# Kernel optimization log

Measured on AMD Instinct MI355X. Metric: run time of the kernel, lower is better.

## Reference

```python
import jax, jax.numpy as jnp
import numpy as np

B, T, D, HD = 8, 2048, 768, 64

def setup_inputs() -> dict:
    key = jax.random.key(0)
    k1, k2, k3, k4 = jax.random.split(key, 4)
    scale = 1.0 / np.sqrt(D)
    return {
        "x": jax.random.normal(k1, (B, T, D), dtype=jnp.float32),
        "Wq": jax.random.normal(k2, (D, HD), dtype=jnp.float32) * scale,
        "Wk": jax.random.normal(k3, (D, HD), dtype=jnp.float32) * scale,
        "Wv": jax.random.normal(k4, (D, HD), dtype=jnp.float32) * scale,
    }

def reference(x, Wq, Wk, Wv):
    # q,k,v: [B,T,HD]
    q = jnp.einsum('btd,dh->bth', x, Wq)
    k = jnp.einsum('btd,dh->bth', x, Wk)
    v = jnp.einsum('btd,dh->bth', x, Wv)
    dk = q.shape[-1]
    # scores: [B,T,T], scaled then causally masked with -inf
    scores = jnp.einsum('bqh,bkh->bqk', q, k) / jnp.sqrt(jnp.float32(dk))
    Tq = scores.shape[-1]
    causal = jnp.tril(jnp.ones((Tq, Tq), dtype=bool))
    scores = jnp.where(causal, scores, -jnp.inf)
    attn = jax.nn.softmax(scores, axis=-1)  # dropout rate 0 (eval mode)
    return jnp.einsum('bqk,bkh->bqh', attn, v)
```

## Files before the change

### kernel.cpp

```cpp
#include <hip/hip_runtime.h>
#include <hip/hip_bf16.h>
#include <stdint.h>

#define B_  8
#define T_  2048
#define D_  768
#define HD_ 64
#define M_  (B_ * T_)

typedef short s16x8 __attribute__((ext_vector_type(8)));
typedef float f32x4 __attribute__((ext_vector_type(4)));
typedef float f32x16 __attribute__((ext_vector_type(16)));
typedef unsigned int u32;

union Frag { uint4 u; s16x8 h; };

__device__ __forceinline__ unsigned short f2bf(float f) {
    unsigned u = __builtin_bit_cast(unsigned, f);
    u += 0x7FFFu + ((u >> 16) & 1u);
    return (unsigned short)(u >> 16);
}
__device__ __forceinline__ unsigned pack_bf16x2(float lo, float hi) {
    return (unsigned)f2bf(lo) | ((unsigned)f2bf(hi) << 16);
}
__device__ __forceinline__ unsigned cvt_pk(float lo, float hi) {
    unsigned r;
    asm("v_cvt_pk_bf16_f32 %0, %1, %2" : "=v"(r) : "v"(lo), "v"(hi));
    return r;
}

__device__ __forceinline__ void gl_lds16(const void* g, void* l) {
    __builtin_amdgcn_global_load_lds(
        (const __attribute__((address_space(1))) u32*)g,
        (__attribute__((address_space(3))) u32*)l, 16, 0, 0);
}

__global__ __launch_bounds__(64) void prep_pk(const float* __restrict__ Wq,
                                              const float* __restrict__ Wk,
                                              const float* __restrict__ Wv,
                                              unsigned short* __restrict__ pk) {
    int nb = blockIdx.x / 24, kk = blockIdx.x % 24;
    int lane = threadIdx.x, g = lane >> 4, t = lane & 15;
    int mat = nb >> 2, col = (nb & 3) * 16 + t;
    const float* W = (mat == 0) ? Wq : (mat == 1) ? Wk : Wv;
    float s = (mat == 0) ? 0.18033688011112042f : 1.0f;
    float v[8];
#pragma unroll
    for (int e = 0; e < 8; e++)
        v[e] = W[(size_t)(kk * 32 + g * 8 + e) * HD_ + col] * s;
    uint4 u;
    u.x = pack_bf16x2(v[0], v[1]);
    u.y = pack_bf16x2(v[2], v[3]);
    u.z = pack_bf16x2(v[4], v[5]);
    u.w = pack_bf16x2(v[6], v[7]);
    *(uint4*)(pk + ((size_t)blockIdx.x * 64 + lane) * 8) = u;
}

__global__ __launch_bounds__(256, 2) void qkv_proj(const float* __restrict__ x,
                                                   const unsigned short* __restrict__ pk,
                                                   unsigned short* __restrict__ qo,
                                                   unsigned short* __restrict__ ko,
                                                   unsigned short* __restrict__ vt) {
    __shared__ char xs[4][8192];

    int tid = threadIdx.x, w = tid >> 6, lane = tid & 63;
    int g = lane >> 4, t = lane & 15;
    int m0 = blockIdx.x * 32;

    auto STAGE = [&](int jb) {
        int buf = jb & 3;
#pragma unroll
        for (int h = 0; h < 2; h++) {
            int s = tid + h * 256;
            int row = s >> 4;
            int a = (s & 15) ^ (row & 15);
            gl_lds16(x + (size_t)(m0 + row) * D_ + jb * 64 + a * 4,
                     &xs[buf][(w * 64 + h * 256) * 16]);
        }
    };

    const unsigned short* wp = pk + (size_t)w * 36864;
    auto LOADB = [&](Frag (&bb)[6], int jb) {
#pragma unroll
        for (int j = 0; j < 3; j++)
#pragma unroll
            for (int c = 0; c < 2; c++)
                bb[j * 2 + c].u = *(const uint4*)(wp + ((size_t)(j * 24 + jb * 2 + c) * 64 + lane) * 8);
    };

    f32x4 acc[3][2];
#pragma unroll
    for (int j = 0; j < 3; j++)
#pragma unroll
        for (int mf = 0; mf < 2; mf++) acc[j][mf] = (f32x4){0.f, 0.f, 0.f, 0.f};

    Frag bfr[3][6];
    LOADB(bfr[0], 0);
    LOADB(bfr[1], 1);
    STAGE(0); STAGE(1); STAGE(2);

#pragma unroll
    for (int jb = 0; jb < 12; jb++) {
        if (jb + 2 < 12) LOADB(bfr[(jb + 2) % 3], jb + 2);
        if (jb == 0)       asm volatile("s_waitcnt vmcnt(10)" ::: "memory");
        else if (jb == 10) asm volatile("s_waitcnt vmcnt(8)"  ::: "memory");
        else if (jb == 11) asm volatile("s_waitcnt vmcnt(0)"  ::: "memory");
        else               asm volatile("s_waitcnt vmcnt(16)" ::: "memory");
        __builtin_amdgcn_s_barrier();
        int buf = jb & 3;

        Frag af[2][2];
#pragma unroll
        for (int mf = 0; mf < 2; mf++) {
            int r32 = mf * 16 + t;
#pragma unroll
            for (int c = 0; c < 2; c++) {
                float4 f0 = *(const float4*)(&xs[buf][r32 * 256 + (((c * 8 + g * 2 + 0) ^ t) * 16)]);
                float4 f1 = *(const float4*)(&xs[buf][r32 * 256 + (((c * 8 + g * 2 + 1) ^ t) * 16)]);
                af[mf][c].u.x = cvt_pk(f0.x, f0.y);
                af[mf][c].u.y = cvt_pk(f0.z, f0.w);
                af[mf][c].u.z = cvt_pk(f1.x, f1.y);
                af[mf][c].u.w = cvt_pk(f1.z, f1.w);
            }
        }
        __builtin_amdgcn_s_setprio(1);
#pragma unroll
        for (int j = 0; j < 3; j++)
#pragma unroll
            for (int c = 0; c < 2; c++) {
                acc[j][0] = __builtin_amdgcn_mfma_f32_16x16x32_bf16(af[0][c].h, bfr[jb % 3][j * 2 + c].h, acc[j][0], 0, 0, 0);
                acc[j][1] = __builtin_amdgcn_mfma_f32_16x16x32_bf16(af[1][c].h, bfr[jb % 3][j * 2 + c].h, acc[j][1], 0, 0, 0);
            }
        __builtin_amdgcn_s_setprio(0);
        __builtin_amdgcn_s_barrier();
        if (jb + 3 < 12) STAGE(jb + 3);
    }

#pragma unroll
    for (int j = 0; j < 3; j++) {
        int nb = w * 3 + j;
        int col = (nb & 3) * 16 + t;
#pragma unroll
        for (int mf = 0; mf < 2; mf++) {
            int row0 = m0 + mf * 16;
            if (nb < 8) {
                unsigned short* dst = (nb < 4) ? qo : ko;
#pragma unroll
                for (int r = 0; r < 4; r++)
                    dst[(size_t)(row0 + g * 4 + r) * HD_ + col] = f2bf(acc[j][mf][r]);
            } else {
                int bb = m0 >> 11;
                int trow = (row0 & 2047) + g * 4;
                uint2 pkk;
                pkk.x = cvt_pk(acc[j][mf][0], acc[j][mf][1]);
                pkk.y = cvt_pk(acc[j][mf][2], acc[j][mf][3]);
                *(uint2*)(vt + (((size_t)(bb * HD_ + col)) << 11) + trow) = pkk;
            }
        }
    }
}

__global__ __launch_bounds__(256) void attn(const unsigned short* __restrict__ qw,
                                            const unsigned short* __restrict__ kw,
                                            const unsigned short* __restrict__ vt,
                                            float* __restrict__ out) {
    __shared__ char smem[65536];

    int tid = threadIdx.x, wv = tid >> 6, lane = tid & 63;
    int hi = lane >> 5, l31 = lane & 31;
    int blk = blockIdx.x;
    int b = blk & 7, idx = blk >> 3;
    int qblk = (idx < 32) ? (63 - idx) : (idx - 32);
    int q0 = qblk * 32;
    int qg = q0 + l31;
    size_t bbase = (size_t)b * T_;
    int nt = qblk + 1;
    int ks = wv;
    int mt = (nt > ks) ? ((nt - ks + 3) >> 2) : 0;

    const unsigned short* kp = kw + bbase * HD_;
    const unsigned short* vp = vt + ((size_t)(b * HD_) << 11);
    char* KV = smem + wv * 16384;

    Frag qf[4];
#pragma unroll
    for (int c = 0; c < 4; c++)
        qf[c].u = *(const uint4*)(qw + (bbase + qg) * HD_ + c * 16 + hi * 8);

    auto STAGE = [&](int j, int buf) {
        int kv0 = j * 32;
#pragma unroll
        for (int q = 0; q < 4; q++) {
            int kr = q * 8 + (lane >> 3);
            int ka = (lane & 7) ^ (kr & 7);
            gl_lds16(kp + (size_t)(kv0 + kr) * HD_ + ka * 8, KV + buf * 4096 + q * 1024);
        }
#pragma unroll
        for (int q = 0; q < 4; q++) {
            int vd = q * 16 + (lane >> 2);
            int va = (lane & 3) ^ (vd & 3) ^ ((vd >> 2) & 3);
            gl_lds16(vp + ((size_t)vd << 11) + kv0 + va * 8, KV + 8192 + buf * 4096 + q * 1024);
        }
    };

    f32x16 o0, o1;
#pragma unroll
    for (int r = 0; r < 16; r++) { o0[r] = 0.f; o1[r] = 0.f; }
    float lacc = 0.f;

    if (mt > 0) STAGE(ks, 0);
    if (mt > 1) STAGE(ks + 4, 1);

#pragma unroll 1
    for (int i = 0; i < mt; i++) {
        if (i + 1 < mt) asm volatile("s_waitcnt vmcnt(8)" ::: "memory");
        else            asm volatile("s_waitcnt vmcnt(0)" ::: "memory");
        int j = ks + 4 * i;
        const char* KB = KV + (i & 1) * 4096;
        const char* VB = KV + 8192 + (i & 1) * 4096;
        int kv0 = j * 32;

        f32x16 st;
#pragma unroll
        for (int r = 0; r < 16; r++) st[r] = 0.f;
        __builtin_amdgcn_s_setprio(1);
#pragma unroll
        for (int c = 0; c < 4; c++) {
            Frag ka;
            ka.u = *(const uint4*)(KB + l31 * 128 + (((c * 2 + hi) ^ (l31 & 7)) * 16));
            st = __builtin_amdgcn_mfma_f32_32x32x16_bf16(ka.h, qf[c].h, st, 0, 0, 0);
        }
        __builtin_amdgcn_s_setprio(0);

        if (j == qblk) {
#pragma unroll
            for (int r = 0; r < 16; r++) {
                int key = kv0 + (r & 3) + 8 * (r >> 2) + 4 * hi;
                if (key > qg) st[r] = -1e30f;
            }
        }

        float p[16], ss = 0.f;
#pragma unroll
        for (int r = 0; r < 16; r++) { p[r] = exp2f(st[r]); ss += p[r]; }
        lacc += ss;

        u32 A0 = cvt_pk(p[0], p[1]),   A1 = cvt_pk(p[2], p[3]);
        u32 B0 = cvt_pk(p[4], p[5]),   B1 = cvt_pk(p[6], p[7]);
        u32 C0 = cvt_pk(p[8], p[9]),   C1 = cvt_pk(p[10], p[11]);
        u32 D0 = cvt_pk(p[12], p[13]), D1 = cvt_pk(p[14], p[15]);
        u32 A0x = (u32)__shfl_xor((int)A0, 32);
        u32 A1x = (u32)__shfl_xor((int)A1, 32);
        u32 B0x = (u32)__shfl_xor((int)B0, 32);
        u32 B1x = (u32)__shfl_xor((int)B1, 32);
        u32 C0x = (u32)__shfl_xor((int)C0, 32);
        u32 C1x = (u32)__shfl_xor((int)C1, 32);
        u32 D0x = (u32)__shfl_xor((int)D0, 32);
        u32 D1x = (u32)__shfl_xor((int)D1, 32);
        Frag pf0, pf1;
        pf0.u.x = hi ? B0x : A0;
        pf0.u.y = hi ? B1x : A1;
        pf0.u.z = hi ? B0  : A0x;
        pf0.u.w = hi ? B1  : A1x;
        pf1.u.x = hi ? D0x : C0;
        pf1.u.y = hi ? D1x : C1;
        pf1.u.z = hi ? D0  : C0x;
        pf1.u.w = hi ? D1  : C1x;

        __builtin_amdgcn_s_setprio(1);
        {
            int sw0 = (l31 & 3) ^ ((l31 >> 2) & 3);
            Frag va;
            va.u = *(const uint4*)(VB + l31 * 64 + (((hi) ^ sw0) * 16));
            o0 = __builtin_amdgcn_mfma_f32_32x32x16_bf16(va.h, pf0.h, o0, 0, 0, 0);
            va.u = *(const uint4*)(VB + l31 * 64 + (((2 + hi) ^ sw0) * 16));
            o0 = __builtin_amdgcn_mfma_f32_32x32x16_bf16(va.h, pf1.h, o0, 0, 0, 0);
            int d1 = 32 + l31;
            int sw1 = (d1 & 3) ^ ((d1 >> 2) & 3);
            va.u = *(const uint4*)(VB + d1 * 64 + (((hi) ^ sw1) * 16));
            o1 = __builtin_amdgcn_mfma_f32_32x32x16_bf16(va.h, pf0.h, o1, 0, 0, 0);
            va.u = *(const uint4*)(VB + d1 * 64 + (((2 + hi) ^ sw1) * 16));
            o1 = __builtin_amdgcn_mfma_f32_32x32x16_bf16(va.h, pf1.h, o1, 0, 0, 0);
        }
        __builtin_amdgcn_s_setprio(0);

        if (i + 2 < mt) STAGE(ks + 4 * (i + 2), i & 1);
    }

    __syncthreads();

    lacc += __shfl_xor(lacc, 32);
    float* MO = (float*)smem;
    if (wv) {
        int base = ((wv - 1) * 64 + lane) * 33;
#pragma unroll
        for (int r = 0; r < 16; r++) { MO[base + r] = o0[r]; MO[base + 16 + r] = o1[r]; }
        MO[base + 32] = lacc;
    }
    __syncthreads();
    if (wv == 0) {
        float ls = lacc;
#pragma unroll
        for (int k = 0; k < 3; k++) ls += MO[(k * 64 + lane) * 33 + 32];
        float inv = 1.0f / ls;
        float* op = out + (bbase + qg) * HD_;
#pragma unroll
        for (int r = 0; r < 16; r++) {
            float s0 = o0[r], s1 = o1[r];
#pragma unroll
            for (int k = 0; k < 3; k++) {
                s0 += MO[(k * 64 + lane) * 33 + r];
                s1 += MO[(k * 64 + lane) * 33 + 16 + r];
            }
            int dr = (r & 3) + 8 * (r >> 2) + 4 * hi;
            op[dr] = s0 * inv;
            op[32 + dr] = s1 * inv;
        }
    }
}

extern "C" void kernel_launch(void* const* d_in, const int* in_sizes, int n_in,
                              void* d_out, int out_size, void* d_ws, size_t ws_size,
                              hipStream_t stream) {
    const float* x  = (const float*)d_in[0];
    const float* Wq = (const float*)d_in[1];
    const float* Wk = (const float*)d_in[2];
    const float* Wv = (const float*)d_in[3];
    char* ws = (char*)d_ws;
    unsigned short* pkw = (unsigned short*)ws;
    unsigned short* qw = (unsigned short*)(ws + 294912);
    unsigned short* kw = (unsigned short*)(ws + 294912 + 2097152);
    unsigned short* vt = (unsigned short*)(ws + 294912 + 4194304);
    float* out = (float*)d_out;

    hipLaunchKernelGGL(prep_pk, dim3(288), dim3(64), 0, stream, Wq, Wk, Wv, pkw);
    hipLaunchKernelGGL(qkv_proj, dim3(M_ / 32), dim3(256), 0, stream, x, pkw, qw, kw, vt);
    hipLaunchKernelGGL(attn, dim3(512), dim3(256), 0, stream, qw, kw, vt, out);
}
```

Before: 45.13 us.

## Unroll the KV loop by two and overlap the next QK MFMA with softmax

The attention loop is split into a QK lambda and a softmax-plus-PV lambda, and the main loop is unrolled by two. The second tile's QK MFMAs are issued before the first tile's softmax and PV, so matrix work can overlap with exp and shuffle work. The single vmcnt wait per tile becomes finer waits that release the K half of each tile before its V half, with a tail path for odd tile counts. In exchange it needs more live registers for the second score tile, which may hurt occupancy, and it relies on the hand-counted vmcnt values staying correct.

```diff
diff --git a/kernel.cpp b/kernel.cpp
--- a/kernel.cpp
+++ b/kernel.cpp
@@ -208,19 +208,7 @@
     for (int r = 0; r < 16; r++) { o0[r] = 0.f; o1[r] = 0.f; }
     float lacc = 0.f;
 
-    if (mt > 0) STAGE(ks, 0);
-    if (mt > 1) STAGE(ks + 4, 1);
-
-#pragma unroll 1
-    for (int i = 0; i < mt; i++) {
-        if (i + 1 < mt) asm volatile("s_waitcnt vmcnt(8)" ::: "memory");
-        else            asm volatile("s_waitcnt vmcnt(0)" ::: "memory");
-        int j = ks + 4 * i;
-        const char* KB = KV + (i & 1) * 4096;
-        const char* VB = KV + 8192 + (i & 1) * 4096;
-        int kv0 = j * 32;
-
-        f32x16 st;
+    auto QK = [&](const char* KB, f32x16& st) {
 #pragma unroll
         for (int r = 0; r < 16; r++) st[r] = 0.f;
         __builtin_amdgcn_s_setprio(1);
@@ -231,7 +219,10 @@
             st = __builtin_amdgcn_mfma_f32_32x32x16_bf16(ka.h, qf[c].h, st, 0, 0, 0);
         }
         __builtin_amdgcn_s_setprio(0);
-
+    };
+
+    auto SMPV = [&](f32x16& st, int j, const char* VB) {
+        int kv0 = j * 32;
         if (j == qblk) {
 #pragma unroll
             for (int r = 0; r < 16; r++) {
@@ -239,7 +230,6 @@
                 if (key > qg) st[r] = -1e30f;
             }
         }
-
         float p[16], ss = 0.f;
 #pragma unroll
         for (int r = 0; r < 16; r++) { p[r] = exp2f(st[r]); ss += p[r]; }
@@ -283,10 +273,44 @@
             o1 = __builtin_amdgcn_mfma_f32_32x32x16_bf16(va.h, pf1.h, o1, 0, 0, 0);
         }
         __builtin_amdgcn_s_setprio(0);
-
+    };
+
+    if (mt > 0) STAGE(ks, 0);
+    if (mt > 1) STAGE(ks + 4, 1);
+
+    int i = 0;
+#pragma unroll 1
+    for (; i + 2 <= mt; i += 2) {
+        int ja = ks + 4 * i, jb2 = ja + 4;
+        const char* KA = KV + (i & 1) * 4096;
+        const char* VA = KV + 8192 + (i & 1) * 4096;
+        const char* KB2 = KV + ((i + 1) & 1) * 4096;
+        const char* VB2 = KV + 8192 + ((i + 1) & 1) * 4096;
+
+        asm volatile("s_waitcnt vmcnt(12)" ::: "memory");
+        f32x16 sa;
+        QK(KA, sa);
+        asm volatile("s_waitcnt vmcnt(4)" ::: "memory");
+        f32x16 sb;
+        QK(KB2, sb);
+        SMPV(sa, ja, VA);
+        asm volatile("s_waitcnt vmcnt(0)" ::: "memory");
         if (i + 2 < mt) STAGE(ks + 4 * (i + 2), i & 1);
-    }
-
+        SMPV(sb, jb2, VB2);
+        if (i + 3 < mt) STAGE(ks + 4 * (i + 3), (i + 1) & 1);
+    }
+    if (i < mt) {
+        int ja = ks + 4 * i;
+        const char* KA = KV + (i & 1) * 4096;
+        const char* VA = KV + 8192 + (i & 1) * 4096;
+        asm volatile("s_waitcnt vmcnt(4)" ::: "memory");
+        f32x16 sa;
+        QK(KA, sa);
+        asm volatile("s_waitcnt vmcnt(0)" ::: "memory");
+        SMPV(sa, ja, VA);
+    }
+
+    asm volatile("s_waitcnt vmcnt(0)" ::: "memory");
     __syncthreads();
 
     lacc += __shfl_xor(lacc, 32);
```

Result: faster. 42.34 us (-6.2%).

## Process 64-query tiles with 8 waves sharing each K/V tile across two query halves

Applied to the files above, without the earlier changes.

The attention kernel now gives each block 64 queries and 8 waves of 512 threads, launching 256 blocks instead of 512. Each staged K/V tile serves two 32-query sub-tiles, halving K/V global loads per query. K and V staging are split so the V prefetch is issued after the PV step. The final cross-wave reduction uses a swizzled float4 shared-memory layout with all threads writing vectorised output. The costs are about 130KB of LDS per block (one block per CU), more registers, fewer blocks, and coarser causal load balance.

```diff
diff --git a/kernel.cpp b/kernel.cpp
--- a/kernel.cpp
+++ b/kernel.cpp
@@ -160,34 +160,35 @@
     }
 }
 
-__global__ __launch_bounds__(256) void attn(const unsigned short* __restrict__ qw,
-                                            const unsigned short* __restrict__ kw,
-                                            const unsigned short* __restrict__ vt,
-                                            float* __restrict__ out) {
-    __shared__ char smem[65536];
+__global__ __launch_bounds__(512, 1) void attn(const unsigned short* __restrict__ qw,
+                                               const unsigned short* __restrict__ kw,
+                                               const unsigned short* __restrict__ vt,
+                                               float* __restrict__ out) {
+    __shared__ char smem[133120];
 
     int tid = threadIdx.x, wv = tid >> 6, lane = tid & 63;
     int hi = lane >> 5, l31 = lane & 31;
     int blk = blockIdx.x;
     int b = blk & 7, idx = blk >> 3;
-    int qblk = (idx < 32) ? (63 - idx) : (idx - 32);
-    int q0 = qblk * 32;
-    int qg = q0 + l31;
+    int qblk = 31 - idx;
+    int q0 = qblk * 64;
+    int qg0 = q0 + l31, qg1 = q0 + 32 + l31;
     size_t bbase = (size_t)b * T_;
-    int nt = qblk + 1;
-    int ks = wv;
-    int mt = (nt > ks) ? ((nt - ks + 3) >> 2) : 0;
+    int nt = 2 * qblk + 2;
+    int mt = (nt > wv) ? ((nt - wv + 7) >> 3) : 0;
 
     const unsigned short* kp = kw + bbase * HD_;
     const unsigned short* vp = vt + ((size_t)(b * HD_) << 11);
     char* KV = smem + wv * 16384;
 
-    Frag qf[4];
-#pragma unroll
-    for (int c = 0; c < 4; c++)
-        qf[c].u = *(const uint4*)(qw + (bbase + qg) * HD_ + c * 16 + hi * 8);
-
-    auto STAGE = [&](int j, int buf) {
+    Frag qf0[4], qf1[4];
+#pragma unroll
+    for (int c = 0; c < 4; c++) {
+        qf0[c].u = *(const uint4*)(qw + (bbase + qg0) * HD_ + c * 16 + hi * 8);
+        qf1[c].u = *(const uint4*)(qw + (bbase + qg1) * HD_ + c * 16 + hi * 8);
+    }
+
+    auto STAGE_K = [&](int j, int buf) {
         int kv0 = j * 32;
 #pragma unroll
         for (int q = 0; q < 4; q++) {
@@ -195,6 +196,9 @@
             int ka = (lane & 7) ^ (kr & 7);
             gl_lds16(kp + (size_t)(kv0 + kr) * HD_ + ka * 8, KV + buf * 4096 + q * 1024);
         }
+    };
+    auto STAGE_V = [&](int j, int buf) {
+        int kv0 = j * 32;
 #pragma unroll
         for (int q = 0; q < 4; q++) {
             int vd = q * 16 + (lane >> 2);
@@ -203,47 +207,25 @@
         }
     };
 
-    f32x16 o0, o1;
-#pragma unroll
-    for (int r = 0; r < 16; r++) { o0[r] = 0.f; o1[r] = 0.f; }
-    float lacc = 0.f;
-
-    if (mt > 0) STAGE(ks, 0);
-    if (mt > 1) STAGE(ks + 4, 1);
-
-#pragma unroll 1
-    for (int i = 0; i < mt; i++) {
-        if (i + 1 < mt) asm volatile("s_waitcnt vmcnt(8)" ::: "memory");
-        else            asm volatile("s_waitcnt vmcnt(0)" ::: "memory");
-        int j = ks + 4 * i;
-        const char* KB = KV + (i & 1) * 4096;
-        const char* VB = KV + 8192 + (i & 1) * 4096;
+    f32x16 o0, o1, o2, o3;
+#pragma unroll
+    for (int r = 0; r < 16; r++) { o0[r] = 0.f; o1[r] = 0.f; o2[r] = 0.f; o3[r] = 0.f; }
+    float l0 = 0.f, l1 = 0.f;
+
+    auto SMPV = [&](f32x16& st, int j, int diagj, int qg,
+                    f32x16& olo, f32x16& ohi, float& lac, const char* VB) {
         int kv0 = j * 32;
-
-        f32x16 st;
-#pragma unroll
-        for (int r = 0; r < 16; r++) st[r] = 0.f;
-        __builtin_amdgcn_s_setprio(1);
-#pragma unroll
-        for (int c = 0; c < 4; c++) {
-            Frag ka;
-            ka.u = *(const uint4*)(KB + l31 * 128 + (((c * 2 + hi) ^ (l31 & 7)) * 16));
-            st = __builtin_amdgcn_mfma_f32_32x32x16_bf16(ka.h, qf[c].h, st, 0, 0, 0);
-        }
-        __builtin_amdgcn_s_setprio(0);
-
-        if (j == qblk) {
+        if (j >= diagj) {
 #pragma unroll
             for (int r = 0; r < 16; r++) {
                 int key = kv0 + (r & 3) + 8 * (r >> 2) + 4 * hi;
                 if (key > qg) st[r] = -1e30f;
             }
         }
-
         float p[16], ss = 0.f;
 #pragma unroll
         for (int r = 0; r < 16; r++) { p[r] = exp2f(st[r]); ss += p[r]; }
-        lacc += ss;
+        lac += ss;
 
         u32 A0 = cvt_pk(p[0], p[1]),   A1 = cvt_pk(p[2], p[3]);
         u32 B0 = cvt_pk(p[4], p[5]),   B1 = cvt_pk(p[6], p[7]);
@@ -272,49 +254,110 @@
             int sw0 = (l31 & 3) ^ ((l31 >> 2) & 3);
             Frag va;
             va.u = *(const uint4*)(VB + l31 * 64 + (((hi) ^ sw0) * 16));
-            o0 = __builtin_amdgcn_mfma_f32_32x32x16_bf16(va.h, pf0.h, o0, 0, 0, 0);
+            olo = __builtin_amdgcn_mfma_f32_32x32x16_bf16(va.h, pf0.h, olo, 0, 0, 0);
             va.u = *(const uint4*)(VB + l31 * 64 + (((2 + hi) ^ sw0) * 16));
-            o0 = __builtin_amdgcn_mfma_f32_32x32x16_bf16(va.h, pf1.h, o0, 0, 0, 0);
+            olo = __builtin_amdgcn_mfma_f32_32x32x16_bf16(va.h, pf1.h, olo, 0, 0, 0);
             int d1 = 32 + l31;
             int sw1 = (d1 & 3) ^ ((d1 >> 2) & 3);
             va.u = *(const uint4*)(VB + d1 * 64 + (((hi) ^ sw1) * 16));
-            o1 = __builtin_amdgcn_mfma_f32_32x32x16_bf16(va.h, pf0.h, o1, 0, 0, 0);
+            ohi = __builtin_amdgcn_mfma_f32_32x32x16_bf16(va.h, pf0.h, ohi, 0, 0, 0);
             va.u = *(const uint4*)(VB + d1 * 64 + (((2 + hi) ^ sw1) * 16));
-            o1 = __builtin_amdgcn_mfma_f32_32x32x16_bf16(va.h, pf1.h, o1, 0, 0, 0);
+            ohi = __builtin_amdgcn_mfma_f32_32x32x16_bf16(va.h, pf1.h, ohi, 0, 0, 0);
         }
         __builtin_amdgcn_s_setprio(0);
-
-        if (i + 2 < mt) STAGE(ks + 4 * (i + 2), i & 1);
-    }
-
+    };
+
+    if (mt > 0) { STAGE_K(wv, 0); STAGE_V(wv, 0); }
+    if (mt > 1) { STAGE_K(wv + 8, 1); STAGE_V(wv + 8, 1); }
+
+#pragma unroll 1
+    for (int i = 0; i < mt; i++) {
+        int j = wv + 8 * i;
+        const char* KB = KV + (i & 1) * 4096;
+        const char* VB = KV + 8192 + (i & 1) * 4096;
+        bool last = (i == mt - 1);
+
+        if (last) asm volatile("s_waitcnt vmcnt(4)"  ::: "memory");
+        else      asm volatile("s_waitcnt vmcnt(12)" ::: "memory");
+
+        Frag ka[4];
+#pragma unroll
+        for (int c = 0; c < 4; c++)
+            ka[c].u = *(const uint4*)(KB + l31 * 128 + (((c * 2 + hi) ^ (l31 & 7)) * 16));
+        f32x16 s0, s1;
+#pragma unroll
+        for (int r = 0; r < 16; r++) { s0[r] = 0.f; s1[r] = 0.f; }
+        __builtin_amdgcn_s_setprio(1);
+#pragma unroll
+        for (int c = 0; c < 4; c++) {
+            s0 = __builtin_amdgcn_mfma_f32_32x32x16_bf16(ka[c].h, qf0[c].h, s0, 0, 0, 0);
+            s1 = __builtin_amdgcn_mfma_f32_32x32x16_bf16(ka[c].h, qf1[c].h, s1, 0, 0, 0);
+        }
+        __builtin_amdgcn_s_setprio(0);
+
+        if (i + 2 < mt) STAGE_K(wv + 8 * (i + 2), i & 1);
+
+        if (last)             asm volatile("s_waitcnt vmcnt(0)"  ::: "memory");
+        else if (i == mt - 2) asm volatile("s_waitcnt vmcnt(8)"  ::: "memory");
+        else                  asm volatile("s_waitcnt vmcnt(12)" ::: "memory");
+
+        SMPV(s0, j, nt - 2, qg0, o0, o1, l0, VB);
+        SMPV(s1, j, nt - 1, qg1, o2, o3, l1, VB);
+
+        if (i + 2 < mt) STAGE_V(wv + 8 * (i + 2), i & 1);
+    }
+
+    asm volatile("s_waitcnt vmcnt(0)" ::: "memory");
+    l0 += __shfl_xor(l0, 32);
+    l1 += __shfl_xor(l1, 32);
     __syncthreads();
 
-    lacc += __shfl_xor(lacc, 32);
-    float* MO = (float*)smem;
-    if (wv) {
-        int base = ((wv - 1) * 64 + lane) * 33;
-#pragma unroll
-        for (int r = 0; r < 16; r++) { MO[base + r] = o0[r]; MO[base + 16 + r] = o1[r]; }
-        MO[base + 32] = lacc;
+    float* MOf = (float*)smem;
+    float* Lb = (float*)(smem + 131072);
+    {
+        int base = wv * 4096 + l31 * 64;
+        f32x16* oarr[4] = { &o0, &o1, &o2, &o3 };
+#pragma unroll
+        for (int sd = 0; sd < 4; sd++) {
+            int sub = sd >> 1, dh = sd & 1;
+            f32x16& oo = *oarr[sd];
+#pragma unroll
+            for (int k4 = 0; k4 < 4; k4++) {
+                int s = dh * 8 + (((hi << 2) | k4) ^ (l31 & 7));
+                float4 q4;
+                q4.x = oo[k4 * 4 + 0]; q4.y = oo[k4 * 4 + 1];
+                q4.z = oo[k4 * 4 + 2]; q4.w = oo[k4 * 4 + 3];
+                *(float4*)&MOf[base + sub * 2048 + s * 4] = q4;
+            }
+        }
+        if (hi == 0) {
+            Lb[wv * 64 + l31] = l0;
+            Lb[wv * 64 + 32 + l31] = l1;
+        }
     }
     __syncthreads();
-    if (wv == 0) {
-        float ls = lacc;
-#pragma unroll
-        for (int k = 0; k < 3; k++) ls += MO[(k * 64 + lane) * 33 + 32];
-        float inv = 1.0f / ls;
-        float* op = out + (bbase + qg) * HD_;
-#pragma unroll
-        for (int r = 0; r < 16; r++) {
-            float s0 = o0[r], s1 = o1[r];
-#pragma unroll
-            for (int k = 0; k < 3; k++) {
-                s0 += MO[(k * 64 + lane) * 33 + r];
-                s1 += MO[(k * 64 + lane) * 33 + 16 + r];
-            }
-            int dr = (r & 3) + 8 * (r >> 2) + 4 * hi;
-            op[dr] = s0 * inv;
-            op[32 + dr] = s1 * inv;
+    {
+        int e0 = tid * 8;
+        int sub = (e0 >> 11) & 1, lq = (e0 >> 6) & 31;
+        float lsum = 0.f;
+#pragma unroll
+        for (int w2 = 0; w2 < 8; w2++) lsum += Lb[w2 * 64 + sub * 32 + lq];
+        float inv = 1.0f / lsum;
+        int row = q0 + sub * 32 + lq;
+        float* op = out + (bbase + row) * HD_;
+#pragma unroll
+        for (int q = 0; q < 2; q++) {
+            int eq = e0 + q * 4;
+            int dh = (eq >> 5) & 1, h2 = (eq >> 4) & 1, r2 = (eq >> 2) & 3;
+            int s = dh * 8 + (((h2 << 2) | r2) ^ (lq & 7));
+            float4 a4 = { 0.f, 0.f, 0.f, 0.f };
+#pragma unroll
+            for (int w2 = 0; w2 < 8; w2++) {
+                float4 v4 = *(const float4*)&MOf[w2 * 4096 + sub * 2048 + lq * 64 + s * 4];
+                a4.x += v4.x; a4.y += v4.y; a4.z += v4.z; a4.w += v4.w;
+            }
+            a4.x *= inv; a4.y *= inv; a4.z *= inv; a4.w *= inv;
+            *(float4*)&op[dh * 32 + 8 * r2 + 4 * h2] = a4;
         }
     }
 }
@@ -335,5 +378,5 @@
 
     hipLaunchKernelGGL(prep_pk, dim3(288), dim3(64), 0, stream, Wq, Wk, Wv, pkw);
     hipLaunchKernelGGL(qkv_proj, dim3(M_ / 32), dim3(256), 0, stream, x, pkw, qw, kw, vt);
-    hipLaunchKernelGGL(attn, dim3(512), dim3(256), 0, stream, qw, kw, vt, out);
-}
+    hipLaunchKernelGGL(attn, dim3(256), dim3(512), 0, stream, qw, kw, vt, out);
+}
```

New measurement: 45.43 us. About the same (+0.7%).
